# Performance work log

Hardware: AMD Instinct MI355X
Metric: run time of the kernel (lower is better)

## Reference

```python
import jax, jax.numpy as jnp
import numpy as np

B, S, D, H, F = 4, 4096, 1024, 16, 4096
CAP = 0.125
ROPE_BASE = 10000.0


def setup_inputs() -> dict:
    key = jax.random.key(0)
    ks = jax.random.split(key, 9)
    scale = 0.02
    x = jax.random.normal(ks[0], (B, S, D), jnp.float32)
    causal = jnp.where(jnp.tril(jnp.ones((S, S), bool)), 0.0, -1e9).astype(jnp.float32)
    attention_mask = jnp.broadcast_to(causal[None, None], (B, 1, S, S))
    position_ids = jnp.broadcast_to(jnp.arange(S, dtype=jnp.int32), (B, S))
    return {
        "x": x,
        "attention_mask": attention_mask,
        "position_ids": position_ids,
        "router_w": jax.random.normal(ks[1], (D, 1), jnp.float32) * scale,
        "router_b": jnp.zeros((1,), jnp.float32),
        "wq": jax.random.normal(ks[2], (D, D), jnp.float32) * scale,
        "wk": jax.random.normal(ks[3], (D, D), jnp.float32) * scale,
        "wv": jax.random.normal(ks[4], (D, D), jnp.float32) * scale,
        "wo": jax.random.normal(ks[5], (D, D), jnp.float32) * scale,
        "w1": jax.random.normal(ks[6], (D, F), jnp.float32) * scale,
        "w2": jax.random.normal(ks[7], (F, D), jnp.float32) * scale,
        "ln1": jnp.ones((D,), jnp.float32),
        "ln2": jnp.ones((D,), jnp.float32),
    }


def rmsnorm(x, g):
    return x * jax.lax.rsqrt(jnp.mean(x * x, -1, keepdims=True) + 1e-6) * g


def rope(t, pos):
    # t: [b, h, n, hd], pos: [b, n]
    hd = t.shape[-1]
    inv = 1.0 / (ROPE_BASE ** (jnp.arange(0, hd, 2, dtype=jnp.float32) / hd))
    f = pos[:, None, :, None].astype(jnp.float32) * inv  # [b,1,n,hd/2]
    emb = jnp.concatenate([f, f], axis=-1)
    cos, sin = jnp.cos(emb), jnp.sin(emb)
    rot = jnp.concatenate([-t[..., hd // 2:], t[..., : hd // 2]], axis=-1)
    return t * cos + rot * sin


def reference(x, attention_mask, position_ids, router_w, router_b,
              wq, wk, wv, wo, w1, w2, ln1, ln2):
    b, s, d = x.shape
    hd = d // H
    # router
    weights = (x @ router_w)[..., 0] + router_b[0]  # [b,s]
    k = int(CAP * s)
    topv, topi = jax.lax.top_k(weights, k)
    thr = topv[:, -1]
    sel_mask = (weights > thr[:, None]).astype(x.dtype)  # selects k-1 tokens/row
    kc = k - 1
    sel_idx = jnp.sort(topi[:, :kc], axis=1)  # preserve sequence order, [b,kc]
    bidx = jnp.arange(b)[:, None]
    # gather selected tokens / positions / weights
    x_sel = x[bidx, sel_idx]                 # [b,kc,d]
    pos_sel = position_ids[bidx, sel_idx]    # [b,kc]
    w_sel = weights[bidx, sel_idx]           # [b,kc]
    m = attention_mask[:, 0]                 # [b,s,s]
    m_sel = m[bidx[:, :, None], sel_idx[:, :, None], sel_idx[:, None, :]]  # [b,kc,kc]
    # transformer block on selected tokens
    hn = rmsnorm(x_sel, ln1)

    def heads(t):
        return t.reshape(b, kc, H, hd).transpose(0, 2, 1, 3)

    q = rope(heads(hn @ wq), pos_sel)
    kk = rope(heads(hn @ wk), pos_sel)
    v = heads(hn @ wv)
    sc = jnp.einsum('bhqd,bhkd->bhqk', q, kk) / np.sqrt(hd).astype(np.float32)
    sc = sc + m_sel[:, None]
    a = jax.nn.softmax(sc, axis=-1)
    o = jnp.einsum('bhqk,bhkd->bhqd', a, v).transpose(0, 2, 1, 3).reshape(b, kc, d) @ wo
    x1 = x_sel + o
    x2 = x1 + jax.nn.gelu(rmsnorm(x1, ln2) @ w1) @ w2
    # weighted scatter back + residual passthrough for unselected tokens
    proc = x2 * w_sel[..., None]
    out = jnp.zeros_like(x).at[bidx, sel_idx].set(proc)
    return out + x * (1.0 - sel_mask)[..., None]
```

## Files before the change

kernel.cpp:

```cpp
#include <hip/hip_runtime.h>

typedef __bf16 bf16;
typedef __bf16 bf16x8 __attribute__((ext_vector_type(8)));
typedef __bf16 bf16x4 __attribute__((ext_vector_type(4)));
typedef float f32x4 __attribute__((ext_vector_type(4)));

#define B_ 4
#define S_ 4096
#define D_ 1024
#define H_ 16
#define HD_ 64
#define F_ 4096
#define KC 512
#define M_ (B_ * KC)

#define GLDS16(gp, lp)                                                        \
    __builtin_amdgcn_global_load_lds(                                         \
        (const __attribute__((address_space(1))) void*)(gp),                  \
        (__attribute__((address_space(3))) void*)(lp), 16, 0, 0)

__global__ __launch_bounds__(256) void prep_kernel(const float* __restrict__ x,
                                                   const float* __restrict__ rw,
                                                   const float* __restrict__ rb,
                                                   float* __restrict__ weights,
                                                   const float* __restrict__ wq, bf16* __restrict__ wqT,
                                                   const float* __restrict__ wk, bf16* __restrict__ wkT,
                                                   const float* __restrict__ wv, bf16* __restrict__ wvT,
                                                   const float* __restrict__ wo, bf16* __restrict__ woT,
                                                   const float* __restrict__ w1, bf16* __restrict__ w1T,
                                                   const float* __restrict__ w2, bf16* __restrict__ w2T) {
    int bid = blockIdx.x;
    if (bid < 4096) {
        int wvv = threadIdx.x >> 6, lane = threadIdx.x & 63;
        int t = bid * 4 + wvv;
        const float* xr = x + (size_t)t * D_;
        float s = 0.f;
        for (int c = 0; c < 4; c++) {
            int off = c * 256 + lane * 4;
            float4 xv = *(const float4*)(xr + off);
            float4 wv4 = *(const float4*)(rw + off);
            s += xv.x * wv4.x + xv.y * wv4.y + xv.z * wv4.z + xv.w * wv4.w;
        }
        for (int m = 32; m; m >>= 1) s += __shfl_down(s, m);
        if (lane == 0) weights[t] = s + rb[0];
        return;
    }
    bid -= 4096;
    const float* in;
    bf16* out;
    int C, R, bx, by;
    if (bid < 1024)      { in = wq; out = wqT; C = 1024; R = 1024; bx = bid & 31; by = bid >> 5; }
    else if (bid < 2048) { int t = bid - 1024; in = wk; out = wkT; C = 1024; R = 1024; bx = t & 31; by = t >> 5; }
    else if (bid < 3072) { int t = bid - 2048; in = wv; out = wvT; C = 1024; R = 1024; bx = t & 31; by = t >> 5; }
    else if (bid < 4096) { int t = bid - 3072; in = wo; out = woT; C = 1024; R = 1024; bx = t & 31; by = t >> 5; }
    else if (bid < 8192) { int t = bid - 4096; in = w1; out = w1T; C = 4096; R = 1024; bx = t & 127; by = t >> 7; }
    else                 { int t = bid - 8192; in = w2; out = w2T; C = 1024; R = 4096; bx = t & 31; by = t >> 5; }
    __shared__ bf16 tile[32][33];
    int tx = threadIdx.x & 31, ty = threadIdx.x >> 5;
    int c0 = bx * 32, r0 = by * 32;
    for (int k = 0; k < 4; k++)
        tile[ty + k * 8][tx] = (bf16)in[(size_t)(r0 + ty + k * 8) * C + c0 + tx];
    __syncthreads();
    for (int k = 0; k < 4; k++)
        out[(size_t)(c0 + ty + k * 8) * R + r0 + tx] = tile[tx][ty + k * 8];
}

__global__ __launch_bounds__(1024) void topk_kernel(const float* __restrict__ weights,
                                                    const int* __restrict__ pos_ids,
                                                    int* __restrict__ sel_idx,
                                                    float* __restrict__ w_sel,
                                                    float* __restrict__ possel,
                                                    float* __restrict__ thr,
                                                    int* __restrict__ invmap) {
    __shared__ unsigned ords[S_];
    __shared__ unsigned hist[16][256];
    __shared__ unsigned wscan[16];
    __shared__ unsigned found[2];
    int b = blockIdx.x, tid = threadIdx.x, wv = tid >> 6, lane = tid & 63;
    const float* wb = weights + (size_t)b * S_;
    for (int i = tid; i < S_; i += 1024) {
        unsigned bits = __float_as_uint(wb[i]);
        ords[i] = (bits & 0x80000000u) ? ~bits : (bits | 0x80000000u);
        invmap[b * S_ + i] = -1;
    }
    unsigned pref = 0, pmask = 0;
    int rank = 512;
    for (int level = 0; level < 4; level++) {
        int shift = 24 - level * 8;
        for (int i = tid; i < 16 * 256; i += 1024) (&hist[0][0])[i] = 0;
        __syncthreads();
        for (int i = tid; i < S_; i += 1024) {
            unsigned o = ords[i];
            if ((o & pmask) == pref) atomicAdd(&hist[wv][(o >> shift) & 255], 1u);
        }
        __syncthreads();
        unsigned val = 0, v = 0;
        if (tid < 256) {
            unsigned s = 0;
            for (int w = 0; w < 16; w++) s += hist[w][255 - tid];
            val = s;
            v = s;
            for (int d = 1; d < 64; d <<= 1) {
                unsigned u = __shfl_up(v, d);
                if (lane >= d) v += u;
            }
            if (lane == 63) wscan[wv] = v;
        }
        __syncthreads();
        if (tid < 256) {
            unsigned woff = 0;
            for (int w = 0; w < wv; w++) woff += wscan[w];
            unsigned Ccnt = v + woff;
            if (val > 0 && Ccnt >= (unsigned)rank && Ccnt - val < (unsigned)rank) {
                found[0] = 255 - (unsigned)tid;
                found[1] = Ccnt - val;
            }
        }
        __syncthreads();
        pref |= found[0] << shift;
        pmask |= 0xffu << shift;
        rank -= (int)found[1];
        __syncthreads();
    }
    unsigned T = pref;
    int need_eq = rank - 1;
    unsigned cnt = 0;
    int i0 = tid * 4;
    unsigned o4[4];
    for (int k = 0; k < 4; k++) {
        unsigned o = ords[i0 + k];
        o4[k] = o;
        cnt += (o > T) ? 1u : 0u;
        cnt += (o == T) ? 0x10000u : 0u;
    }
    unsigned v2 = cnt;
    for (int d = 1; d < 64; d <<= 1) {
        unsigned u = __shfl_up(v2, d);
        if (lane >= d) v2 += u;
    }
    if (lane == 63) wscan[wv] = v2;
    __syncthreads();
    unsigned woff2 = 0;
    for (int w = 0; w < wv; w++) woff2 += wscan[w];
    unsigned excl = woff2 + v2 - cnt;
    unsigned gbe = excl & 0xffffu, ebe = excl >> 16;
    for (int k = 0; k < 4; k++) {
        unsigned o = o4[k];
        bool gt = o > T, eq = (o == T);
        if (gt || (eq && ebe < (unsigned)need_eq)) {
            unsigned esel = (ebe < (unsigned)need_eq) ? ebe : (unsigned)need_eq;
            unsigned pos = gbe + esel;
            sel_idx[b * KC + pos] = i0 + k;
            w_sel[b * KC + pos] = wb[i0 + k];
            possel[b * KC + pos] = (float)pos_ids[b * S_ + i0 + k];
            invmap[b * S_ + i0 + k] = (int)pos;
        }
        gbe += gt ? 1u : 0u;
        ebe += eq ? 1u : 0u;
    }
    if (tid == 0) {
        unsigned bits = (T & 0x80000000u) ? (T & 0x7fffffffu) : ~T;
        thr[b] = __uint_as_float(bits);
        sel_idx[b * KC + 511] = 0;
        w_sel[b * KC + 511] = 0.0f;
        possel[b * KC + 511] = 0.0f;
    }
}

__global__ __launch_bounds__(256) void gather_norm_kernel(const float* __restrict__ x,
                                                          const int* __restrict__ sel_idx,
                                                          const float* __restrict__ ln1,
                                                          bf16* __restrict__ hn) {
    int r = blockIdx.x, b = r >> 9, j = r & (KC - 1);
    int tid = threadIdx.x;
    bf16* outr = hn + (size_t)r * D_;
    if (j == 511) {
        ((uint2*)outr)[tid] = make_uint2(0u, 0u);
        return;
    }
    int idx = sel_idx[r];
    const float* xr = x + ((size_t)b * S_ + idx) * D_;
    float4 xv = ((const float4*)xr)[tid];
    float v[4] = {xv.x, xv.y, xv.z, xv.w}, ss = 0.f;
    for (int i = 0; i < 4; i++) ss += v[i] * v[i];
    __shared__ float red[4];
    float t = ss;
    for (int m = 32; m; m >>= 1) t += __shfl_down(t, m);
    if ((tid & 63) == 0) red[tid >> 6] = t;
    __syncthreads();
    ss = red[0] + red[1] + red[2] + red[3];
    float scale = rsqrtf(ss * (1.0f / D_) + 1e-6f);
    float4 lv = ((const float4*)ln1)[tid];
    float lg[4] = {lv.x, lv.y, lv.z, lv.w};
    bf16x4 o;
    for (int i = 0; i < 4; i++) o[i] = (bf16)(v[i] * scale * lg[i]);
    ((bf16x4*)outr)[tid] = o;
}

template <bool GELU, bool ROPE, typename OUT>
__global__ __launch_bounds__(256) void gemm_bt(const bf16* __restrict__ A,
                                               const bf16* __restrict__ B0,
                                               const bf16* __restrict__ B1,
                                               const bf16* __restrict__ B2,
                                               OUT* __restrict__ C, int K, int lda,
                                               int N, int mat_shift,
                                               const float* __restrict__ possel) {
    __shared__ bf16 As[3][128 * 32];
    __shared__ bf16 Bs[3][128 * 32];
    int tid = threadIdx.x;
    int m0 = blockIdx.y * 128, n0 = blockIdx.x * 128;
    int kz = blockIdx.z * K;
    int wave = tid >> 6, lane = tid & 63, quad = lane >> 4, l16 = lane & 15;
    int wm = (wave >> 1) * 64, wn = (wave & 1) * 64;
    int mat = n0 >> mat_shift;
    const bf16* bp = (mat == 0) ? B0 : ((mat == 1) ? B1 : B2);
    int nb = n0 - (mat << mat_shift);
    int r0 = tid >> 2;
    int ksw = ((tid & 3) ^ ((tid >> 3) & 3)) * 8;
    const bf16* a0 = A + (size_t)(m0 + r0) * lda + kz + ksw;
    const bf16* a1 = A + (size_t)(m0 + r0 + 64) * lda + kz + ksw;
    const bf16* bq0 = bp + (size_t)(nb + r0) * lda + kz + ksw;
    const bf16* bq1 = bp + (size_t)(nb + r0 + 64) * lda + kz + ksw;
    int nk = K >> 5;
#define STAGE_T(buf, kk)                                                      \
    do {                                                                      \
        int ks = (kk) << 5;                                                   \
        GLDS16(a0 + ks, &As[buf][tid * 8]);                                   \
        GLDS16(a1 + ks, &As[buf][2048 + tid * 8]);                            \
        GLDS16(bq0 + ks, &Bs[buf][tid * 8]);                                  \
        GLDS16(bq1 + ks, &Bs[buf][2048 + tid * 8]);                           \
    } while (0)
    STAGE_T(0, 0);
    STAGE_T(1, 1);
    f32x4 acc[4][4] = {};
    int qsw = (quad ^ ((l16 >> 1) & 3)) * 8;
    int cur = 0, pf = 2;
    for (int t = 0; t < nk; t++) {
        if (t + 2 < nk) {
            STAGE_T(pf, t + 2);
            asm volatile("s_waitcnt vmcnt(8)\n\ts_barrier" ::: "memory");
        } else if (t + 1 < nk) {
            asm volatile("s_waitcnt vmcnt(4)\n\ts_barrier" ::: "memory");
        } else {
            asm volatile("s_waitcnt vmcnt(0)\n\ts_barrier" ::: "memory");
        }
        const bf16* Ac = &As[cur][0];
        const bf16* Bc = &Bs[cur][0];
        bf16x8 af[4], bfr[4];
        for (int tt = 0; tt < 4; tt++)
            af[tt] = *(const bf16x8*)(Ac + (wm + tt * 16 + l16) * 32 + qsw);
        for (int tt = 0; tt < 4; tt++)
            bfr[tt] = *(const bf16x8*)(Bc + (wn + tt * 16 + l16) * 32 + qsw);
        for (int tm = 0; tm < 4; tm++)
            for (int tn = 0; tn < 4; tn++)
                acc[tm][tn] = __builtin_amdgcn_mfma_f32_16x16x32_bf16(af[tm], bfr[tn], acc[tm][tn], 0, 0, 0);
        asm volatile("s_barrier" ::: "memory");
        cur = (cur == 2) ? 0 : cur + 1;
        pf = (pf == 2) ? 0 : pf + 1;
    }
#undef STAGE_T
    if (ROPE && n0 < 2048) {
        float inv0 = expf(-0.28782313662425572f * (float)l16);
        float inv1 = expf(-0.28782313662425572f * (float)(16 + l16));
        for (int tm = 0; tm < 4; tm++)
            for (int r = 0; r < 4; r++) {
                int rowg = m0 + wm + tm * 16 + quad * 4 + r;
                float pos = possel[rowg];
                {
                    float f = pos * inv0, cs = cosf(f), sn = sinf(f);
                    float lo = acc[tm][0][r], hi = acc[tm][2][r];
                    acc[tm][0][r] = lo * cs - hi * sn;
                    acc[tm][2][r] = hi * cs + lo * sn;
                }
                {
                    float f = pos * inv1, cs = cosf(f), sn = sinf(f);
                    float lo = acc[tm][1][r], hi = acc[tm][3][r];
                    acc[tm][1][r] = lo * cs - hi * sn;
                    acc[tm][3][r] = hi * cs + lo * sn;
                }
            }
    }
    C += (size_t)blockIdx.z * 2048 * N;
    for (int tm = 0; tm < 4; tm++)
        for (int tn = 0; tn < 4; tn++) {
            int col = n0 + wn + tn * 16 + l16;
            for (int r = 0; r < 4; r++) {
                int row = m0 + wm + tm * 16 + quad * 4 + r;
                float v = acc[tm][tn][r];
                if (GELU) {
                    float x3 = v * v * v;
                    v = 0.5f * v * (1.f + tanhf(0.7978845608028654f * (v + 0.044715f * x3)));
                }
                C[(size_t)row * N + col] = (OUT)v;
            }
        }
}

__global__ __launch_bounds__(256) void attn_kernel(const bf16* __restrict__ qkv,
                                                   bf16* __restrict__ O) {
    __shared__ bf16 Qs[64 * 72];
    __shared__ bf16 Ks[128 * 72];
    __shared__ bf16 Vts[64 * 136];
    __shared__ bf16 Ps[64 * 136];
    int bh = blockIdx.y, qt = blockIdx.x;
    int bb = bh >> 4, hh = bh & 15;
    int q_base = qt * 64;
    int tid = threadIdx.x, wave = tid >> 6, lane = tid & 63, quad = lane >> 4, l16 = lane & 15;
    const bf16* qg = qkv + ((size_t)(bb * KC + q_base)) * 3072 + hh * HD_;
    for (int i = 0; i < 2; i++) {
        int c = tid * 2 + i, row = c >> 3, ko = (c & 7) * 8;
        *(uint4*)(Qs + row * 72 + ko) = *(const uint4*)(qg + (size_t)row * 3072 + ko);
    }
    f32x4 oacc[4] = {};
    float mrow[4], lrow[4];
    for (int r = 0; r < 4; r++) { mrow[r] = -1e30f; lrow[r] = 0.f; }
    int kt_max = (q_base + 63) >> 7;
    for (int kt = 0; kt <= kt_max; kt++) {
        __syncthreads();
        const bf16* kg = qkv + ((size_t)(bb * KC + kt * 128)) * 3072 + D_ + hh * HD_;
        for (int i = 0; i < 4; i++) {
            int c = tid * 4 + i, row = c >> 3, ko = (c & 7) * 8;
            *(uint4*)(Ks + row * 72 + ko) = *(const uint4*)(kg + (size_t)row * 3072 + ko);
        }
        const bf16* vbase = qkv + ((size_t)(bb * KC + kt * 128)) * 3072 + 2 * D_ + hh * HD_;
        for (int p = 0; p < 4; p++) {
            int jj = p * 32 + (tid >> 3), ko = (tid & 7) * 8;
            bf16x8 vv = *(const bf16x8*)(vbase + (size_t)jj * 3072 + ko);
            for (int e = 0; e < 8; e++) Vts[(ko + e) * 136 + jj] = vv[e];
        }
        __syncthreads();
        f32x4 sacc[8] = {};
        for (int kk = 0; kk < 2; kk++) {
            bf16x8 aq = *(const bf16x8*)(Qs + (wave * 16 + l16) * 72 + kk * 32 + quad * 8);
            for (int tn = 0; tn < 8; tn++) {
                bf16x8 bk = *(const bf16x8*)(Ks + (tn * 16 + l16) * 72 + kk * 32 + quad * 8);
                sacc[tn] = __builtin_amdgcn_mfma_f32_16x16x32_bf16(aq, bk, sacc[tn], 0, 0, 0);
            }
        }
        for (int r = 0; r < 4; r++) {
            int qi = q_base + wave * 16 + quad * 4 + r;
            float sv[8], mx = -1e30f;
            for (int tn = 0; tn < 8; tn++) {
                int kj = kt * 128 + tn * 16 + l16;
                float s = sacc[tn][r] * 0.125f;
                if (kj > qi) s = -1e30f;
                sv[tn] = s;
                mx = fmaxf(mx, s);
            }
            for (int m = 1; m < 16; m <<= 1) mx = fmaxf(mx, __shfl_xor(mx, m));
            float mnew = fmaxf(mrow[r], mx);
            float alpha = __expf(mrow[r] - mnew);
            float rs = 0.f;
            for (int tn = 0; tn < 8; tn++) {
                float pv = __expf(sv[tn] - mnew);
                rs += pv;
                Ps[(wave * 16 + quad * 4 + r) * 136 + tn * 16 + l16] = (bf16)pv;
            }
            for (int m = 1; m < 16; m <<= 1) rs += __shfl_xor(rs, m);
            lrow[r] = lrow[r] * alpha + rs;
            mrow[r] = mnew;
            for (int tn = 0; tn < 4; tn++) oacc[tn][r] *= alpha;
        }
        __syncthreads();
        for (int kk = 0; kk < 4; kk++) {
            bf16x8 ap = *(const bf16x8*)(Ps + (wave * 16 + l16) * 136 + kk * 32 + quad * 8);
            for (int tn = 0; tn < 4; tn++) {
                bf16x8 bv = *(const bf16x8*)(Vts + (tn * 16 + l16) * 136 + kk * 32 + quad * 8);
                oacc[tn] = __builtin_amdgcn_mfma_f32_16x16x32_bf16(ap, bv, oacc[tn], 0, 0, 0);
            }
        }
    }
    for (int tn = 0; tn < 4; tn++)
        for (int r = 0; r < 4; r++) {
            int rowg = bb * KC + q_base + wave * 16 + quad * 4 + r;
            int col = hh * HD_ + tn * 16 + l16;
            O[(size_t)rowg * D_ + col] = (bf16)(oacc[tn][r] / lrow[r]);
        }
}

__global__ __launch_bounds__(256) void x1norm_kernel(const float* __restrict__ x,
                                                     const bf16* __restrict__ wo_out,
                                                     const int* __restrict__ sel_idx,
                                                     const float* __restrict__ ln2,
                                                     bf16* __restrict__ h_in) {
    int r = blockIdx.x, b = r >> 9;
    int idx = sel_idx[r];
    int tid = threadIdx.x;
    const float* xr = x + ((size_t)b * S_ + idx) * D_;
    float4 xv = ((const float4*)xr)[tid];
    bf16x4 ov = ((const bf16x4*)(wo_out + (size_t)r * D_))[tid];
    float v[4] = {xv.x + (float)ov[0], xv.y + (float)ov[1], xv.z + (float)ov[2], xv.w + (float)ov[3]};
    float ss = 0.f;
    for (int i = 0; i < 4; i++) ss += v[i] * v[i];
    __shared__ float red[4];
    float t = ss;
    for (int m = 32; m; m >>= 1) t += __shfl_down(t, m);
    if ((tid & 63) == 0) red[tid >> 6] = t;
    __syncthreads();
    ss = red[0] + red[1] + red[2] + red[3];
    float scale = rsqrtf(ss * (1.0f / D_) + 1e-6f);
    float4 lv = ((const float4*)ln2)[tid];
    float lg[4] = {lv.x, lv.y, lv.z, lv.w};
    bf16x4 o;
    for (int i = 0; i < 4; i++) o[i] = (bf16)(v[i] * scale * lg[i]);
    ((bf16x4*)(h_in + (size_t)r * D_))[tid] = o;
}

__global__ __launch_bounds__(256) void out_fused_kernel(const float* __restrict__ x,
                                                        const bf16* __restrict__ wo_out,
                                                        const float* __restrict__ f2a,
                                                        const float* __restrict__ f2b,
                                                        const int* __restrict__ invmap,
                                                        const float* __restrict__ weights,
                                                        const float* __restrict__ thr,
                                                        const float* __restrict__ w_sel,
                                                        float* __restrict__ out) {
    int t = blockIdx.x;
    int b = t >> 12;
    int tid = threadIdx.x;
    float w = weights[t];
    float th = thr[b];
    float4 xv = ((const float4*)(x + (size_t)t * D_))[tid];
    float4 res;
    if (w > th) { res.x = 0.f; res.y = 0.f; res.z = 0.f; res.w = 0.f; }
    else res = xv;
    int j = invmap[t];
    if (j >= 0) {
        int r = b * KC + j;
        bf16x4 wv = ((const bf16x4*)(wo_out + (size_t)r * D_))[tid];
        float4 va = ((const float4*)(f2a + (size_t)r * D_))[tid];
        float4 vb = ((const float4*)(f2b + (size_t)r * D_))[tid];
        float ws = w_sel[r];
        res.x += ((xv.x + (float)wv[0]) + (va.x + vb.x)) * ws;
        res.y += ((xv.y + (float)wv[1]) + (va.y + vb.y)) * ws;
        res.z += ((xv.z + (float)wv[2]) + (va.z + vb.z)) * ws;
        res.w += ((xv.w + (float)wv[3]) + (va.w + vb.w)) * ws;
    }
    ((float4*)(out + (size_t)t * D_))[tid] = res;
}

extern "C" void kernel_launch(void* const* d_in, const int* in_sizes, int n_in,
                              void* d_out, int out_size, void* d_ws, size_t ws_size,
                              hipStream_t stream) {
    const float* x = (const float*)d_in[0];
    const int* pos_ids = (const int*)d_in[2];
    const float* rw = (const float*)d_in[3];
    const float* rb = (const float*)d_in[4];
    const float* wq = (const float*)d_in[5];
    const float* wk = (const float*)d_in[6];
    const float* wv = (const float*)d_in[7];
    const float* wo = (const float*)d_in[8];
    const float* w1 = (const float*)d_in[9];
    const float* w2 = (const float*)d_in[10];
    const float* ln1 = (const float*)d_in[11];
    const float* ln2 = (const float*)d_in[12];
    float* out = (float*)d_out;
    (void)in_sizes; (void)n_in; (void)out_size;

    constexpr size_t MB = 1ull << 20;
    char* scr = (ws_size >= 88 * MB) ? (char*)d_ws : (char*)d_in[1];
    float* weights = (float*)(scr + 0);
    float* thr     = (float*)(scr + 0x10000);
    int*   sel     = (int*)  (scr + 0x14000);
    float* wsel    = (float*)(scr + 0x18000);
    float* possel  = (float*)(scr + 0x1A000);
    int*   invmap  = (int*)  (scr + 0x20000);
    bf16*  hn      = (bf16*) (scr + 1 * MB);
    bf16*  wqT     = (bf16*) (scr + 5 * MB);
    bf16*  wkT     = (bf16*) (scr + 7 * MB);
    bf16*  wvT     = (bf16*) (scr + 9 * MB);
    bf16*  qkv     = (bf16*) (scr + 11 * MB);
    bf16*  obuf    = (bf16*) (scr + 23 * MB);
    bf16*  woT     = (bf16*) (scr + 27 * MB);
    bf16*  wo_out  = (bf16*) (scr + 29 * MB);
    bf16*  h_in    = (bf16*) (scr + 33 * MB);
    bf16*  w1T     = (bf16*) (scr + 37 * MB);
    bf16*  h1      = (bf16*) (scr + 45 * MB);
    bf16*  w2T     = (bf16*) (scr + 61 * MB);
    float* f2a     = (float*)(scr + 69 * MB);
    float* f2b     = (float*)(scr + 77 * MB);

    prep_kernel<<<dim3(16384), 256, 0, stream>>>(x, rw, rb, weights,
                                                 wq, wqT, wk, wkT, wv, wvT,
                                                 wo, woT, w1, w1T, w2, w2T);
    topk_kernel<<<dim3(B_), 1024, 0, stream>>>(weights, pos_ids, sel, wsel, possel, thr, invmap);
    gather_norm_kernel<<<dim3(M_), 256, 0, stream>>>(x, sel, ln1, hn);
    gemm_bt<false, true, bf16><<<dim3(24, 16), 256, 0, stream>>>(hn, wqT, wkT, wvT, qkv,
                                                                 1024, 1024, 3 * D_, 10, possel);
    attn_kernel<<<dim3(8, B_ * H_), 256, 0, stream>>>(qkv, obuf);
    gemm_bt<false, false, bf16><<<dim3(8, 16), 256, 0, stream>>>(obuf, woT, woT, woT, wo_out,
                                                                 1024, 1024, D_, 10, nullptr);
    x1norm_kernel<<<dim3(M_), 256, 0, stream>>>(x, wo_out, sel, ln2, h_in);
    gemm_bt<true, false, bf16><<<dim3(32, 16), 256, 0, stream>>>(h_in, w1T, w1T, w1T, h1,
                                                                 1024, 1024, F_, 12, nullptr);
    gemm_bt<false, false, float><<<dim3(8, 16, 2), 256, 0, stream>>>(h1, w2T, w2T, w2T, f2a,
                                                                     2048, 4096, D_, 10, nullptr);
    out_fused_kernel<<<dim3(B_ * S_), 256, 0, stream>>>(x, wo_out, f2a, f2b, invmap,
                                                        weights, thr, wsel, out);
}
```

Before: 600.2 us.

## Remap GEMM blocks across XCDs and shrink attention key tiles with swizzled V

GEMM blocks are remapped so that consecutive hardware block IDs, which round-robin over the 8 XCDs, land on contiguous tiles within each XCD. This is meant to improve L2 reuse of the A and B operands. The attention kernel now uses 64-key tiles instead of 128, which cuts masked causal work on diagonal tiles and shrinks shared memory. It also switches to a flat 1D grid with bh in the low bits and adds an XOR swizzle on the transposed V store to reduce LDS bank conflicts. The cost is more loop iterations, and therefore more barriers, per attention block.

```diff
diff --git a/kernel.cpp b/kernel.cpp
--- a/kernel.cpp
+++ b/kernel.cpp
@@ -207,9 +207,17 @@
                                                const float* __restrict__ possel) {
     __shared__ bf16 As[3][128 * 32];
     __shared__ bf16 Bs[3][128 * 32];
+    unsigned h = blockIdx.x + gridDim.x * (blockIdx.y + gridDim.y * blockIdx.z);
+    unsigned Nb = gridDim.x * gridDim.y * gridDim.z;
+    unsigned cpx = Nb >> 3;
+    unsigned L = (h & 7) * cpx + (h >> 3);
+    unsigned by = L & 15;
+    unsigned rest = L >> 4;
+    unsigned bxu = rest % gridDim.x;
+    unsigned bzu = rest / gridDim.x;
+    int m0 = by * 128, n0 = bxu * 128;
+    int kz = bzu * K;
     int tid = threadIdx.x;
-    int m0 = blockIdx.y * 128, n0 = blockIdx.x * 128;
-    int kz = blockIdx.z * K;
     int wave = tid >> 6, lane = tid & 63, quad = lane >> 4, l16 = lane & 15;
     int wm = (wave >> 1) * 64, wn = (wave & 1) * 64;
     int mat = n0 >> mat_shift;
@@ -280,7 +288,7 @@
                 }
             }
     }
-    C += (size_t)blockIdx.z * 2048 * N;
+    C += (size_t)bzu * 2048 * N;
     for (int tm = 0; tm < 4; tm++)
         for (int tn = 0; tn < 4; tn++) {
             int col = n0 + wn + tn * 16 + l16;
@@ -299,10 +307,12 @@
 __global__ __launch_bounds__(256) void attn_kernel(const bf16* __restrict__ qkv,
                                                    bf16* __restrict__ O) {
     __shared__ bf16 Qs[64 * 72];
-    __shared__ bf16 Ks[128 * 72];
-    __shared__ bf16 Vts[64 * 136];
-    __shared__ bf16 Ps[64 * 136];
-    int bh = blockIdx.y, qt = blockIdx.x;
+    __shared__ bf16 Ks[64 * 72];
+    __shared__ bf16 Vts[64 * 72];
+    __shared__ bf16 Ps[64 * 72];
+    int bid = blockIdx.x;
+    int bh = bid & 63;
+    int qt = ((bid >> 6) & 3) | ((bid >> 8) << 2);
     int bb = bh >> 4, hh = bh & 15;
     int q_base = qt * 64;
     int tid = threadIdx.x, wave = tid >> 6, lane = tid & 63, quad = lane >> 4, l16 = lane & 15;
@@ -314,34 +324,34 @@
     f32x4 oacc[4] = {};
     float mrow[4], lrow[4];
     for (int r = 0; r < 4; r++) { mrow[r] = -1e30f; lrow[r] = 0.f; }
-    int kt_max = (q_base + 63) >> 7;
-    for (int kt = 0; kt <= kt_max; kt++) {
-        __syncthreads();
-        const bf16* kg = qkv + ((size_t)(bb * KC + kt * 128)) * 3072 + D_ + hh * HD_;
-        for (int i = 0; i < 4; i++) {
-            int c = tid * 4 + i, row = c >> 3, ko = (c & 7) * 8;
+    for (int kt = 0; kt <= qt; kt++) {
+        __syncthreads();
+        const bf16* kg = qkv + ((size_t)(bb * KC + kt * 64)) * 3072 + D_ + hh * HD_;
+        for (int i = 0; i < 2; i++) {
+            int c = tid * 2 + i, row = c >> 3, ko = (c & 7) * 8;
             *(uint4*)(Ks + row * 72 + ko) = *(const uint4*)(kg + (size_t)row * 3072 + ko);
         }
-        const bf16* vbase = qkv + ((size_t)(bb * KC + kt * 128)) * 3072 + 2 * D_ + hh * HD_;
-        for (int p = 0; p < 4; p++) {
+        const bf16* vbase = qkv + ((size_t)(bb * KC + kt * 64)) * 3072 + 2 * D_ + hh * HD_;
+        for (int p = 0; p < 2; p++) {
             int jj = p * 32 + (tid >> 3), ko = (tid & 7) * 8;
             bf16x8 vv = *(const bf16x8*)(vbase + (size_t)jj * 3072 + ko);
-            for (int e = 0; e < 8; e++) Vts[(ko + e) * 136 + jj] = vv[e];
-        }
-        __syncthreads();
-        f32x4 sacc[8] = {};
+            int colp = (((jj >> 3) ^ (tid & 7)) << 3) | (jj & 7);
+            for (int e = 0; e < 8; e++) Vts[(ko + e) * 72 + colp] = vv[e];
+        }
+        __syncthreads();
+        f32x4 sacc[4] = {};
         for (int kk = 0; kk < 2; kk++) {
             bf16x8 aq = *(const bf16x8*)(Qs + (wave * 16 + l16) * 72 + kk * 32 + quad * 8);
-            for (int tn = 0; tn < 8; tn++) {
+            for (int tn = 0; tn < 4; tn++) {
                 bf16x8 bk = *(const bf16x8*)(Ks + (tn * 16 + l16) * 72 + kk * 32 + quad * 8);
                 sacc[tn] = __builtin_amdgcn_mfma_f32_16x16x32_bf16(aq, bk, sacc[tn], 0, 0, 0);
             }
         }
         for (int r = 0; r < 4; r++) {
             int qi = q_base + wave * 16 + quad * 4 + r;
-            float sv[8], mx = -1e30f;
-            for (int tn = 0; tn < 8; tn++) {
-                int kj = kt * 128 + tn * 16 + l16;
+            float sv[4], mx = -1e30f;
+            for (int tn = 0; tn < 4; tn++) {
+                int kj = kt * 64 + tn * 16 + l16;
                 float s = sacc[tn][r] * 0.125f;
                 if (kj > qi) s = -1e30f;
                 sv[tn] = s;
@@ -351,10 +361,10 @@
             float mnew = fmaxf(mrow[r], mx);
             float alpha = __expf(mrow[r] - mnew);
             float rs = 0.f;
-            for (int tn = 0; tn < 8; tn++) {
+            for (int tn = 0; tn < 4; tn++) {
                 float pv = __expf(sv[tn] - mnew);
                 rs += pv;
-                Ps[(wave * 16 + quad * 4 + r) * 136 + tn * 16 + l16] = (bf16)pv;
+                Ps[(wave * 16 + quad * 4 + r) * 72 + tn * 16 + l16] = (bf16)pv;
             }
             for (int m = 1; m < 16; m <<= 1) rs += __shfl_xor(rs, m);
             lrow[r] = lrow[r] * alpha + rs;
@@ -362,10 +372,12 @@
             for (int tn = 0; tn < 4; tn++) oacc[tn][r] *= alpha;
         }
         __syncthreads();
-        for (int kk = 0; kk < 4; kk++) {
-            bf16x8 ap = *(const bf16x8*)(Ps + (wave * 16 + l16) * 136 + kk * 32 + quad * 8);
+        for (int kk = 0; kk < 2; kk++) {
+            bf16x8 ap = *(const bf16x8*)(Ps + (wave * 16 + l16) * 72 + kk * 32 + quad * 8);
             for (int tn = 0; tn < 4; tn++) {
-                bf16x8 bv = *(const bf16x8*)(Vts + (tn * 16 + l16) * 136 + kk * 32 + quad * 8);
+                int d = tn * 16 + l16;
+                int colb = (((kk * 4 + quad) ^ ((d >> 3) & 7)) << 3);
+                bf16x8 bv = *(const bf16x8*)(Vts + d * 72 + colb);
                 oacc[tn] = __builtin_amdgcn_mfma_f32_16x16x32_bf16(ap, bv, oacc[tn], 0, 0, 0);
             }
         }
@@ -487,7 +499,7 @@
     gather_norm_kernel<<<dim3(M_), 256, 0, stream>>>(x, sel, ln1, hn);
     gemm_bt<false, true, bf16><<<dim3(24, 16), 256, 0, stream>>>(hn, wqT, wkT, wvT, qkv,
                                                                  1024, 1024, 3 * D_, 10, possel);
-    attn_kernel<<<dim3(8, B_ * H_), 256, 0, stream>>>(qkv, obuf);
+    attn_kernel<<<dim3(512), 256, 0, stream>>>(qkv, obuf);
     gemm_bt<false, false, bf16><<<dim3(8, 16), 256, 0, stream>>>(obuf, woT, woT, woT, wo_out,
                                                                  1024, 1024, D_, 10, nullptr);
     x1norm_kernel<<<dim3(M_), 256, 0, stream>>>(x, wo_out, sel, ln2, h_in);
```

Measured after the change: 591.5 us. Within noise of the previous version (-1.4%).
